# Kernel tuning notes

Hardware: AMD Instinct MI355X
Metric: run time of the kernel (lower is better)

The kernel has to match this reference:

```python
import jax, jax.numpy as jnp
from jax import lax
import numpy as np

B, C, O, H, W = 4, 64, 64, 128, 128


def setup_inputs() -> dict:
    key = jax.random.key(0)
    ks = jax.random.split(key, 3)
    x = jax.random.normal(ks[0], (B, C, H, W), dtype=jnp.float32)
    # small offset-conv weights so learned offsets stay in a realistic +-few-pixel range
    offset_w = jax.random.normal(ks[1], (27, C, 3, 3), dtype=jnp.float32) * 0.01
    offset_b = jnp.zeros((27,), dtype=jnp.float32)
    dcn_w = jax.random.normal(ks[2], (O, C, 3, 3), dtype=jnp.float32) * (1.0 / np.sqrt(C * 9))
    dcn_b = jnp.zeros((O,), dtype=jnp.float32)
    gamma = jnp.ones((O,), dtype=jnp.float32)
    beta = jnp.zeros((O,), dtype=jnp.float32)
    return {"x": x, "offset_w": offset_w, "offset_b": offset_b,
            "dcn_w": dcn_w, "dcn_b": dcn_b, "gamma": gamma, "beta": beta}


def _bilinear_sample(img, y, x):
    """img: [B,C,H,W]; y,x: [B,K,H,W] fractional coords. Returns [B,C,K,H,W].
    Out-of-range corners contribute 0 (DCNv2 semantics)."""
    Bs, Cs, Hs, Ws = img.shape
    flat = img.reshape(Bs, Cs, Hs * Ws)
    y0 = jnp.floor(y)
    x0 = jnp.floor(x)
    wy = y - y0
    wx = x - x0

    def gather(yi, xi):
        valid = (yi >= 0) & (yi <= Hs - 1) & (xi >= 0) & (xi <= Ws - 1)
        yc = jnp.clip(yi, 0, Hs - 1).astype(jnp.int32)
        xc = jnp.clip(xi, 0, Ws - 1).astype(jnp.int32)
        idx = (yc * Ws + xc).reshape(Bs, -1)  # [B, K*H*W]
        v = jax.vmap(lambda f, i: jnp.take(f, i, axis=1))(flat, idx)  # [B,C,K*H*W]
        v = v.reshape(Bs, Cs, *y.shape[1:])
        return v * valid[:, None].astype(img.dtype)

    out = jnp.zeros((Bs, Cs) + y.shape[1:], dtype=img.dtype)
    for dy, dx in ((0, 0), (0, 1), (1, 0), (1, 1)):
        w = (wy if dy else 1.0 - wy) * (wx if dx else 1.0 - wx)
        out = out + gather(y0 + dy, x0 + dx) * w[:, None]
    return out


def reference(x, offset_w, offset_b, dcn_w, dcn_b, gamma, beta):
    Bs, Cs, Hs, Ws = x.shape
    Os = dcn_w.shape[0]
    # offset-predicting 3x3 conv, stride 1, pad 1
    om = lax.conv_general_dilated(
        x, offset_w, window_strides=(1, 1), padding=((1, 1), (1, 1)),
        dimension_numbers=("NCHW", "OIHW", "NCHW")) + offset_b[None, :, None, None]
    off_x, off_y, mask = jnp.split(om, 3, axis=1)  # each [B,9,H,W]
    mask = jax.nn.sigmoid(mask)

    # base sampling grid: p0 + kernel tap offset (stride 1, pad 1, dil 1)
    ky, kx = jnp.meshgrid(jnp.arange(3), jnp.arange(3), indexing="ij")
    kyf = ky.reshape(9).astype(x.dtype)
    kxf = kx.reshape(9).astype(x.dtype)
    hh = jnp.arange(Hs, dtype=x.dtype)
    ww = jnp.arange(Ws, dtype=x.dtype)
    py = hh[None, None, :, None] - 1.0 + kyf[None, :, None, None] + off_y  # [B,9,H,W]
    px = ww[None, None, None, :] - 1.0 + kxf[None, :, None, None] + off_x  # [B,9,H,W]

    sampled = _bilinear_sample(x, py, px)          # [B,C,9,H,W]
    sampled = sampled * mask[:, None]              # sigmoid modulation
    out = jnp.einsum("bckhw,ock->bohw", sampled, dcn_w.reshape(Os, Cs, 9))
    out = out + dcn_b[None, :, None, None]

    # BatchNorm (training-mode batch stats) + ReLU
    mu = out.mean(axis=(0, 2, 3), keepdims=True)
    var = out.var(axis=(0, 2, 3), keepdims=True)
    out = (out - mu) * lax.rsqrt(var + 1e-5)
    out = out * gamma[None, :, None, None] + beta[None, :, None, None]
    return jax.nn.relu(out)
```

## Files before the change

### kernel.cpp

```cpp
#include <hip/hip_runtime.h>
#include <math.h>

#define Hh 128
#define Ww 128
#define HW (Hh*Ww)
#define Bn 4
#define Cn 64
#define On 64
#define KP 200
#define OMP 66
#define NBLK 1024

typedef __attribute__((ext_vector_type(8))) short bf16x8;
typedef __attribute__((ext_vector_type(4))) float f32x4;
typedef __attribute__((ext_vector_type(4))) unsigned short u16x4;
typedef __attribute__((ext_vector_type(4))) short s16x4;

static __device__ __forceinline__ unsigned short f2bf(float f) {
    unsigned u = __builtin_bit_cast(unsigned, f);
    u += 0x7FFFu + ((u >> 16) & 1u);
    return (unsigned short)(u >> 16);
}
static __device__ __forceinline__ float bf2f(unsigned short s) {
    unsigned u = ((unsigned)s) << 16;
    return __builtin_bit_cast(float, u);
}
static __device__ __forceinline__ short f2h(float f) {
    _Float16 h = (_Float16)f;
    return __builtin_bit_cast(short, h);
}
static __device__ __forceinline__ float h2f(short s) {
    return (float)__builtin_bit_cast(_Float16, s);
}

#define XTB_BYTES   ((size_t)Bn*HW*64*2)
#define CONV_BYTES  ((size_t)Bn*On*HW*4)
#define PART_BYTES  ((size_t)128*NBLK*4)

__global__ __launch_bounds__(256) void prep_k(
    const float* __restrict__ x,  const float* __restrict__ ow,
    const float* __restrict__ dw, unsigned* __restrict__ xtb,
    short* __restrict__ owT,      short* __restrict__ dwT)
{
    int blk = blockIdx.x;
    int t = threadIdx.x;
    if (blk < 512) {
        int b = blk >> 7, h = blk & 127;
        __shared__ float sT[64 * 133];
        const float* xp = x + (size_t)b * Cn * HW + (size_t)h * Ww;
#pragma unroll
        for (int it = 0; it < 32; ++it) {
            int idx = t + 256 * it;
            int c = idx >> 7, w = idx & 127;
            sT[c * 133 + w] = xp[(size_t)c * HW + w];
        }
        __syncthreads();
        unsigned* op = xtb + (size_t)blk * Ww * 32;
#pragma unroll
        for (int it = 0; it < 16; ++it) {
            int idx = t + 256 * it;
            int w = idx >> 5, cp = idx & 31;
            unsigned lo = f2bf(sT[(2 * cp) * 133 + w]);
            unsigned hi = f2bf(sT[(2 * cp + 1) * 133 + w]);
            op[(size_t)w * 32 + cp] = lo | (hi << 16);
        }
    } else {
        int u = (blk - 512) * 4 + (t >> 6);
        int c = t & 63;
        if (u < 288) {
            int o = u / 9, kk = u % 9;
            float v = (o < 27) ? ow[(size_t)o * 576 + c * 9 + kk] : 0.0f;
            owT[(size_t)u * 64 + c] = (short)f2bf(v);
        } else {
            int u2 = u - 288;
            int o = u2 / 9, kk = u2 % 9;
            dwT[(size_t)u2 * 64 + c] = (short)f2bf(dw[(size_t)o * 576 + c * 9 + kk]);
        }
    }
}

__global__ __launch_bounds__(256) void dcn_fused_k(
    const unsigned* __restrict__ xtb, const short* __restrict__ owT,
    const float* __restrict__ ob,     const short* __restrict__ dwT,
    float* __restrict__ conv,         float* __restrict__ part)
{
    int raw  = blockIdx.x;
    int blk  = ((raw & 7) << 7) | (raw >> 3);
    int half = blk & 1;
    int h    = (blk >> 1) & 127;
    int b    = blk >> 8;
    int px0  = half * 64;
    int t    = threadIdx.x;
    int lane = t & 63;
    int quad = lane >> 4;
    int l15  = lane & 15;
    int hl   = lane >> 5;
    int cl   = lane & 31;
    int w_s  = __builtin_amdgcn_readfirstlane(t >> 6);

    __shared__ __align__(16) short sA[64 * KP];
    __shared__ __align__(16) short sOMh[27 * OMP + 12];
    __shared__ __align__(16) unsigned short prepIdx[576 * 4];
    __shared__ __align__(16) short prepW[576 * 4];

    const unsigned* xbd = xtb + (size_t)b * HW * 32;
    unsigned* sAd = (unsigned*)sA;

    int nt_o = w_s & 1;
    int mh   = w_s >> 1;
    int o_ow = nt_o * 16 + l15;
    f32x4 oacc[2] = {{0,0,0,0},{0,0,0,0}};

    for (int ck = 0; ck < 3; ++ck) {
#pragma unroll 4
        for (int pr = 0; pr < 24; ++pr) {
            int pair = pr * 4 + w_s;
            int kkl = pair >> 5, px2 = pair & 31;
            int px = px2 * 2 + hl;
            int yy = h + ck - 1;
            int xx = px0 + px + kkl - 1;
            bool valid = ((unsigned)yy < (unsigned)Hh) && ((unsigned)xx < (unsigned)Ww);
            unsigned v = valid ? xbd[(((size_t)yy << 7) + xx) * 32 + cl] : 0u;
            sAd[px * 100 + kkl * 32 + cl] = v;
        }
        __syncthreads();
#pragma unroll
        for (int ks = 0; ks < 6; ++ks) {
            int kk = ck * 3 + (ks >> 1);
            bf16x8 bfr = *(const bf16x8*)&owT[((size_t)o_ow * 9 + kk) * 64
                                             + (ks & 1) * 32 + quad * 8];
#pragma unroll
            for (int m2 = 0; m2 < 2; ++m2) {
                bf16x8 a = *(const bf16x8*)&sA[(mh * 32 + m2 * 16 + l15) * KP
                                               + ks * 32 + quad * 8];
                oacc[m2] = __builtin_amdgcn_mfma_f32_16x16x32_bf16(a, bfr, oacc[m2], 0, 0, 0);
            }
        }
        __syncthreads();
    }
    if (o_ow < 27) {
        float bias = ob[o_ow];
#pragma unroll
        for (int m2 = 0; m2 < 2; ++m2) {
            int pxb = (mh * 2 + m2) * 16 + quad * 4;
#pragma unroll
            for (int r = 0; r < 4; ++r)
                sOMh[o_ow * OMP + pxb + r] = f2h(oacc[m2][r] + bias);
        }
    }
    __syncthreads();

#pragma unroll
    for (int i = 0; i < 3; ++i) {
        int u = t + 256 * i;
        if (u < 576) {
            int kk = u >> 6, px = u & 63;
            float ox = h2f(sOMh[kk * OMP + px]);
            float oy = h2f(sOMh[(9 + kk) * OMP + px]);
            float mr = h2f(sOMh[(18 + kk) * OMP + px]);
            float m  = 1.0f / (1.0f + __expf(-mr));
            float py  = (float)(h - 1 + (kk / 3)) + oy;
            float pxf = (float)(px0 + px - 1 + (kk % 3)) + ox;
            float y0f = floorf(py), x0f = floorf(pxf);
            int y0 = (int)y0f, x0 = (int)x0f;
            float wy = py - y0f, wx = pxf - x0f;
#pragma unroll
            for (int dy = 0; dy < 2; ++dy) {
#pragma unroll
                for (int dx = 0; dx < 2; ++dx) {
                    int yi = y0 + dy, xi = x0 + dx;
                    bool valid = (yi >= 0) && (yi < Hh) && (xi >= 0) && (xi < Ww);
                    int yc = min(max(yi, 0), Hh - 1);
                    int xc = min(max(xi, 0), Ww - 1);
                    float wgt = (dy ? wy : 1.0f - wy) * (dx ? wx : 1.0f - wx);
                    prepIdx[u * 4 + dy * 2 + dx] = (unsigned short)(yc * Ww + xc);
                    prepW[u * 4 + dy * 2 + dx]   = f2h(valid ? (wgt * m) : 0.0f);
                }
            }
        }
    }
    __syncthreads();

    int o_dw = w_s * 16 + l15;
    f32x4 acc[4] = {{0,0,0,0},{0,0,0,0},{0,0,0,0},{0,0,0,0}};

    for (int ck = 0; ck < 3; ++ck) {
#pragma unroll 4
        for (int uu = 0; uu < 24; ++uu) {
            int unit = (uu * 4 + w_s) * 2 + hl;
            int kkl = unit >> 6, px = unit & 63;
            int u = ck * 192 + unit;
            u16x4 pi = *(const u16x4*)&prepIdx[u * 4];
            s16x4 pw = *(const s16x4*)&prepW[u * 4];
            float v0 = 0.0f, v1 = 0.0f;
#pragma unroll
            for (int j = 0; j < 4; ++j) {
                unsigned d = xbd[(size_t)pi[j] * 32 + cl];
                float wj = h2f(pw[j]);
                float clo = __builtin_bit_cast(float, d << 16);
                float chi = __builtin_bit_cast(float, d & 0xFFFF0000u);
                v0 += wj * clo;
                v1 += wj * chi;
            }
            unsigned pk;
            asm("v_cvt_pk_bf16_f32 %0, %1, %2" : "=v"(pk) : "v"(v0), "v"(v1));
            sAd[px * 100 + kkl * 32 + cl] = pk;
        }
        __syncthreads();
#pragma unroll
        for (int ks = 0; ks < 6; ++ks) {
            int kk = ck * 3 + (ks >> 1);
            bf16x8 bfr = *(const bf16x8*)&dwT[((size_t)o_dw * 9 + kk) * 64
                                              + (ks & 1) * 32 + quad * 8];
#pragma unroll
            for (int mt = 0; mt < 4; ++mt) {
                bf16x8 a = *(const bf16x8*)&sA[(mt * 16 + l15) * KP
                                               + ks * 32 + quad * 8];
                acc[mt] = __builtin_amdgcn_mfma_f32_16x16x32_bf16(a, bfr, acc[mt], 0, 0, 0);
            }
        }
        __syncthreads();
    }

#pragma unroll
    for (int mt = 0; mt < 4; ++mt) {
        size_t idx = ((size_t)b * On + o_dw) * HW + (size_t)h * Ww + px0 + mt * 16 + quad * 4;
        *(f32x4*)(conv + idx) = acc[mt];
    }
    float s1 = 0.0f, s2 = 0.0f;
#pragma unroll
    for (int mt = 0; mt < 4; ++mt) {
#pragma unroll
        for (int r = 0; r < 4; ++r) {
            float v = acc[mt][r];
            s1 += v;
            s2 += v * v;
        }
    }
    s1 += __shfl_down(s1, 32, 64);  s2 += __shfl_down(s2, 32, 64);
    s1 += __shfl_down(s1, 16, 64);  s2 += __shfl_down(s2, 16, 64);
    if (lane < 16) {
        part[(size_t)o_dw * NBLK + blk]        = s1;
        part[(size_t)(64 + o_dw) * NBLK + blk] = s2;
    }
}

__global__ __launch_bounds__(256) void stats_k(
    const float* __restrict__ part, const float* __restrict__ gamma,
    const float* __restrict__ beta, float* __restrict__ ss)
{
    int o = blockIdx.x;
    int t = threadIdx.x;
    float s1 = 0.0f, s2 = 0.0f;
    for (int i = t; i < NBLK; i += 256) {
        s1 += part[(size_t)o * NBLK + i];
        s2 += part[(size_t)(64 + o) * NBLK + i];
    }
#pragma unroll
    for (int off = 32; off > 0; off >>= 1) {
        s1 += __shfl_down(s1, off, 64);
        s2 += __shfl_down(s2, off, 64);
    }
    __shared__ float r1[4], r2[4];
    if ((t & 63) == 0) { r1[t >> 6] = s1; r2[t >> 6] = s2; }
    __syncthreads();
    if (t == 0) {
        float S1 = r1[0] + r1[1] + r1[2] + r1[3];
        float S2 = r2[0] + r2[1] + r2[2] + r2[3];
        float n = (float)(Bn * HW);
        float mu = S1 / n;
        float var = S2 / n - mu * mu;
        float sc = gamma[o] * rsqrtf(var + 1e-5f);
        ss[o] = sc;
        ss[64 + o] = beta[o] - mu * sc;
    }
}

__global__ __launch_bounds__(256) void bnrelu_k(
    const float* __restrict__ conv, const float* __restrict__ ss,
    float* __restrict__ out)
{
    int i = blockIdx.x * blockDim.x + threadIdx.x;
    int ch = (i >> 12) & 63;
    float sc = ss[ch];
    float sh = ss[64 + ch];
    const float4* cv = (const float4*)conv;
    float4* ov = (float4*)out;
    float4 v = cv[i];
    v.x = fmaxf(v.x * sc + sh, 0.0f);
    v.y = fmaxf(v.y * sc + sh, 0.0f);
    v.z = fmaxf(v.z * sc + sh, 0.0f);
    v.w = fmaxf(v.w * sc + sh, 0.0f);
    ov[i] = v;
}

extern "C" void kernel_launch(void* const* d_in, const int* in_sizes, int n_in,
                              void* d_out, int out_size, void* d_ws, size_t ws_size,
                              hipStream_t stream)
{
    const float* x     = (const float*)d_in[0];
    const float* ow    = (const float*)d_in[1];
    const float* ob    = (const float*)d_in[2];
    const float* dw    = (const float*)d_in[3];
    const float* gamma = (const float*)d_in[5];
    const float* beta  = (const float*)d_in[6];

    char* wsb = (char*)d_ws;
    unsigned* xtb = (unsigned*)wsb;
    float* conv = (float*)(wsb + XTB_BYTES);
    float* part = (float*)(wsb + XTB_BYTES + CONV_BYTES);
    float* ss   = (float*)(wsb + XTB_BYTES + CONV_BYTES + PART_BYTES);
    short* owT  = (short*)(wsb + XTB_BYTES + CONV_BYTES + PART_BYTES + 512);
    short* dwT  = owT + 288 * 64;

    prep_k     <<<dim3(728),  dim3(256), 0, stream>>>(x, ow, dw, xtb, owT, dwT);
    dcn_fused_k<<<dim3(NBLK), dim3(256), 0, stream>>>(xtb, owT, ob, dwT, conv, part);
    stats_k    <<<dim3(64),   dim3(256), 0, stream>>>(part, gamma, beta, ss);
    bnrelu_k   <<<dim3(Bn * On * HW / 4 / 256), dim3(256), 0, stream>>>(conv, ss, (float*)d_out);
}
```

Before: 139.5 us.

## Fuse BN stats into BN-ReLU pass and use base-index bilinear corner addressing

Merges the stats kernel and the BN+ReLU kernel into one launch. Each of 1024 blocks recomputes its channel's reduction over the partial sums, then normalizes a 16K-element slice. In the DCN kernel the four bilinear corner indices become one clamped base index plus fixed offsets, with the weights adjusted so edge cases stay correct. The offset/mask staging buffer now aliases the sA tile buffer to cut LDS use. The trade-off is redundant reduction work per block and somewhat more setup arithmetic per sample.

```diff
diff --git a/kernel.cpp b/kernel.cpp
--- a/kernel.cpp
+++ b/kernel.cpp
@@ -14,16 +14,11 @@
 typedef __attribute__((ext_vector_type(8))) short bf16x8;
 typedef __attribute__((ext_vector_type(4))) float f32x4;
 typedef __attribute__((ext_vector_type(4))) unsigned short u16x4;
-typedef __attribute__((ext_vector_type(4))) short s16x4;
 
 static __device__ __forceinline__ unsigned short f2bf(float f) {
     unsigned u = __builtin_bit_cast(unsigned, f);
     u += 0x7FFFu + ((u >> 16) & 1u);
     return (unsigned short)(u >> 16);
-}
-static __device__ __forceinline__ float bf2f(unsigned short s) {
-    unsigned u = ((unsigned)s) << 16;
-    return __builtin_bit_cast(float, u);
 }
 static __device__ __forceinline__ short f2h(float f) {
     _Float16 h = (_Float16)f;
@@ -99,9 +94,9 @@
     int w_s  = __builtin_amdgcn_readfirstlane(t >> 6);
 
     __shared__ __align__(16) short sA[64 * KP];
-    __shared__ __align__(16) short sOMh[27 * OMP + 12];
-    __shared__ __align__(16) unsigned short prepIdx[576 * 4];
-    __shared__ __align__(16) short prepW[576 * 4];
+    __shared__ __align__(16) unsigned short prepQ[576 * 4];
+    __shared__ __align__(16) unsigned short prepC[576];
+    short* sOMh = sA;
 
     const unsigned* xbd = xtb + (size_t)b * HW * 32;
     unsigned* sAd = (unsigned*)sA;
@@ -155,28 +150,27 @@
         int u = t + 256 * i;
         if (u < 576) {
             int kk = u >> 6, px = u & 63;
-            float ox = h2f(sOMh[kk * OMP + px]);
-            float oy = h2f(sOMh[(9 + kk) * OMP + px]);
-            float mr = h2f(sOMh[(18 + kk) * OMP + px]);
+            float ox = h2f((short)sOMh[kk * OMP + px]);
+            float oy = h2f((short)sOMh[(9 + kk) * OMP + px]);
+            float mr = h2f((short)sOMh[(18 + kk) * OMP + px]);
             float m  = 1.0f / (1.0f + __expf(-mr));
             float py  = (float)(h - 1 + (kk / 3)) + oy;
             float pxf = (float)(px0 + px - 1 + (kk % 3)) + ox;
             float y0f = floorf(py), x0f = floorf(pxf);
             int y0 = (int)y0f, x0 = (int)x0f;
             float wy = py - y0f, wx = pxf - x0f;
-#pragma unroll
-            for (int dy = 0; dy < 2; ++dy) {
-#pragma unroll
-                for (int dx = 0; dx < 2; ++dx) {
-                    int yi = y0 + dy, xi = x0 + dx;
-                    bool valid = (yi >= 0) && (yi < Hh) && (xi >= 0) && (xi < Ww);
-                    int yc = min(max(yi, 0), Hh - 1);
-                    int xc = min(max(xi, 0), Ww - 1);
-                    float wgt = (dy ? wy : 1.0f - wy) * (dx ? wx : 1.0f - wx);
-                    prepIdx[u * 4 + dy * 2 + dx] = (unsigned short)(yc * Ww + xc);
-                    prepW[u * 4 + dy * 2 + dx]   = f2h(valid ? (wgt * m) : 0.0f);
-                }
-            }
+            int yb = min(max(y0, 0), Hh - 2);
+            int xb = min(max(x0, 0), Ww - 2);
+            float wr0 = (yb == y0) ? (1.0f - wy) : ((yb     == y0 + 1) ? wy : 0.0f);
+            float wr1 = (yb == y0) ? wy          : ((yb + 1 == y0    ) ? (1.0f - wy) : 0.0f);
+            float wc0 = (xb == x0) ? (1.0f - wx) : ((xb     == x0 + 1) ? wx : 0.0f);
+            float wc1 = (xb == x0) ? wx          : ((xb + 1 == x0    ) ? (1.0f - wx) : 0.0f);
+            wr0 *= m; wr1 *= m;
+            prepQ[u * 4 + 0] = (unsigned short)(yb * Ww + xb);
+            prepQ[u * 4 + 1] = (unsigned short)f2h(wr0 * wc0);
+            prepQ[u * 4 + 2] = (unsigned short)f2h(wr0 * wc1);
+            prepQ[u * 4 + 3] = (unsigned short)f2h(wr1 * wc0);
+            prepC[u]         = (unsigned short)f2h(wr1 * wc1);
         }
     }
     __syncthreads();
@@ -190,18 +184,24 @@
             int unit = (uu * 4 + w_s) * 2 + hl;
             int kkl = unit >> 6, px = unit & 63;
             int u = ck * 192 + unit;
-            u16x4 pi = *(const u16x4*)&prepIdx[u * 4];
-            s16x4 pw = *(const s16x4*)&prepW[u * 4];
-            float v0 = 0.0f, v1 = 0.0f;
-#pragma unroll
-            for (int j = 0; j < 4; ++j) {
-                unsigned d = xbd[(size_t)pi[j] * 32 + cl];
-                float wj = h2f(pw[j]);
-                float clo = __builtin_bit_cast(float, d << 16);
-                float chi = __builtin_bit_cast(float, d & 0xFFFF0000u);
-                v0 += wj * clo;
-                v1 += wj * chi;
-            }
+            u16x4 q = *(const u16x4*)&prepQ[u * 4];
+            float w00 = h2f((short)q[1]);
+            float w01 = h2f((short)q[2]);
+            float w10 = h2f((short)q[3]);
+            float w11 = h2f((short)prepC[u]);
+            const unsigned* p0 = xbd + (size_t)q[0] * 32 + cl;
+            unsigned d00 = p0[0];
+            unsigned d01 = p0[32];
+            unsigned d10 = p0[4096];
+            unsigned d11 = p0[4128];
+            float v0 = w00 * __builtin_bit_cast(float, d00 << 16)
+                     + w01 * __builtin_bit_cast(float, d01 << 16)
+                     + w10 * __builtin_bit_cast(float, d10 << 16)
+                     + w11 * __builtin_bit_cast(float, d11 << 16);
+            float v1 = w00 * __builtin_bit_cast(float, d00 & 0xFFFF0000u)
+                     + w01 * __builtin_bit_cast(float, d01 & 0xFFFF0000u)
+                     + w10 * __builtin_bit_cast(float, d10 & 0xFFFF0000u)
+                     + w11 * __builtin_bit_cast(float, d11 & 0xFFFF0000u);
             unsigned pk;
             asm("v_cvt_pk_bf16_f32 %0, %1, %2" : "=v"(pk) : "v"(v0), "v"(v1));
             sAd[px * 100 + kkl * 32 + cl] = pk;
@@ -245,16 +245,21 @@
     }
 }
 
-__global__ __launch_bounds__(256) void stats_k(
+__global__ __launch_bounds__(256) void bnstats_k(
     const float* __restrict__ part, const float* __restrict__ gamma,
-    const float* __restrict__ beta, float* __restrict__ ss)
+    const float* __restrict__ beta, const float* __restrict__ conv,
+    float* __restrict__ out)
 {
-    int o = blockIdx.x;
+    int idx = blockIdx.x;
+    int o  = idx & 63;
+    int bq = idx >> 6;
     int t = threadIdx.x;
     float s1 = 0.0f, s2 = 0.0f;
-    for (int i = t; i < NBLK; i += 256) {
-        s1 += part[(size_t)o * NBLK + i];
-        s2 += part[(size_t)(64 + o) * NBLK + i];
+#pragma unroll
+    for (int i = 0; i < NBLK / 256; ++i) {
+        int j = t + 256 * i;
+        s1 += part[(size_t)o * NBLK + j];
+        s2 += part[(size_t)(64 + o) * NBLK + j];
     }
 #pragma unroll
     for (int off = 32; off > 0; off >>= 1) {
@@ -262,6 +267,7 @@
         s2 += __shfl_down(s2, off, 64);
     }
     __shared__ float r1[4], r2[4];
+    __shared__ float sc_s, sh_s;
     if ((t & 63) == 0) { r1[t >> 6] = s1; r2[t >> 6] = s2; }
     __syncthreads();
     if (t == 0) {
@@ -271,27 +277,23 @@
         float mu = S1 / n;
         float var = S2 / n - mu * mu;
         float sc = gamma[o] * rsqrtf(var + 1e-5f);
-        ss[o] = sc;
-        ss[64 + o] = beta[o] - mu * sc;
-    }
-}
-
-__global__ __launch_bounds__(256) void bnrelu_k(
-    const float* __restrict__ conv, const float* __restrict__ ss,
-    float* __restrict__ out)
-{
-    int i = blockIdx.x * blockDim.x + threadIdx.x;
-    int ch = (i >> 12) & 63;
-    float sc = ss[ch];
-    float sh = ss[64 + ch];
-    const float4* cv = (const float4*)conv;
-    float4* ov = (float4*)out;
-    float4 v = cv[i];
-    v.x = fmaxf(v.x * sc + sh, 0.0f);
-    v.y = fmaxf(v.y * sc + sh, 0.0f);
-    v.z = fmaxf(v.z * sc + sh, 0.0f);
-    v.w = fmaxf(v.w * sc + sh, 0.0f);
-    ov[i] = v;
+        sc_s = sc;
+        sh_s = beta[o] - mu * sc;
+    }
+    __syncthreads();
+    float sc = sc_s, sh = sh_s;
+    size_t base = (((size_t)(bq >> 2) * On + o) * HW + (size_t)(bq & 3) * 4096) / 4;
+    const float4* cv = (const float4*)conv + base;
+    float4* ov = (float4*)out + base;
+#pragma unroll
+    for (int i = 0; i < 4; ++i) {
+        float4 v = cv[t + 256 * i];
+        v.x = fmaxf(v.x * sc + sh, 0.0f);
+        v.y = fmaxf(v.y * sc + sh, 0.0f);
+        v.z = fmaxf(v.z * sc + sh, 0.0f);
+        v.w = fmaxf(v.w * sc + sh, 0.0f);
+        ov[t + 256 * i] = v;
+    }
 }
 
 extern "C" void kernel_launch(void* const* d_in, const int* in_sizes, int n_in,
@@ -309,12 +311,10 @@
     unsigned* xtb = (unsigned*)wsb;
     float* conv = (float*)(wsb + XTB_BYTES);
     float* part = (float*)(wsb + XTB_BYTES + CONV_BYTES);
-    float* ss   = (float*)(wsb + XTB_BYTES + CONV_BYTES + PART_BYTES);
     short* owT  = (short*)(wsb + XTB_BYTES + CONV_BYTES + PART_BYTES + 512);
     short* dwT  = owT + 288 * 64;
 
     prep_k     <<<dim3(728),  dim3(256), 0, stream>>>(x, ow, dw, xtb, owT, dwT);
     dcn_fused_k<<<dim3(NBLK), dim3(256), 0, stream>>>(xtb, owT, ob, dwT, conv, part);
-    stats_k    <<<dim3(64),   dim3(256), 0, stream>>>(part, gamma, beta, ss);
-    bnrelu_k   <<<dim3(Bn * On * HW / 4 / 256), dim3(256), 0, stream>>>(conv, ss, (float*)d_out);
-}
+    bnstats_k  <<<dim3(1024), dim3(256), 0, stream>>>(part, gamma, beta, conv, (float*)d_out);
+}
```

Result: no change. 136.8 us (-1.9%).
